# Optimization experiments

Measured on AMD Instinct MI355X. Metric: run time of the kernel, lower is better.

## Reference

```python
import jax, jax.numpy as jnp
import numpy as np

BN_EPS = 1e-5
ALPHA = 0.3
NEG = -9e9
BN_SCALE = 1.0 / np.sqrt(1.0 + BN_EPS)  # eval BatchNorm with running_mean=0, running_var=1


def gat_layer(x, mask, W, a, bn_g, bn_b, concat):
    # x: [B,N,Fin], mask: [B,N,N] bool, W: [Fin,Fo], a: [2*Fo]
    h = jnp.einsum('bnf,fo->bno', x, W)               # [B,N,Fo]
    Fo = W.shape[1]
    s1 = h @ a[:Fo]                                    # [B,N]
    s2 = h @ a[Fo:]                                    # [B,N]
    # additive decomposition of concat([h_i, h_j]) @ a (identical math)
    e = jax.nn.leaky_relu(s1[:, :, None] + s2[:, None, :], ALPHA)  # [B,N,N]
    att = jax.nn.softmax(jnp.where(mask, e, NEG), axis=-1)
    hp = jnp.einsum('bnm,bmo->bno', att, h)            # [B,N,Fo]
    # BatchNorm1d(nodes_num) in eval mode, per-node-channel affine
    hp = hp * BN_SCALE * bn_g[None, :, None] + bn_b[None, :, None]
    return jax.nn.elu(hp) if concat else hp


def setup_inputs() -> dict:
    key = jax.random.key(0)
    ks = jax.random.split(key, 10)
    B, N, F, Fo, H, C = 128, 200, 768, 32, 8, 2
    Fh = Fo * H
    return {
        'feat_matrix': jax.random.normal(ks[0], (B, N, F), jnp.float32),
        'adj': jax.random.randint(ks[1], (B, N, N), 0, 2, jnp.int32),
        'W_heads': jax.random.normal(ks[2], (H, F, Fo), jnp.float32) * 0.05,
        'a_heads': jax.random.normal(ks[3], (H, 2 * Fo), jnp.float32) * 0.1,
        'bnh_g': jnp.ones((H, N), jnp.float32),
        'bnh_b': jnp.zeros((H, N), jnp.float32),
        'bnt_g': jnp.ones((N,), jnp.float32),
        'bnt_b': jnp.zeros((N,), jnp.float32),
        'W_sent': jax.random.normal(ks[4], (Fh, C), jnp.float32) * 0.1,
        'a_sent': jax.random.normal(ks[5], (2 * C,), jnp.float32) * 0.1,
        'bns_g': jnp.ones((N,), jnp.float32),
        'bns_b': jnp.zeros((N,), jnp.float32),
        'W_para': jax.random.normal(ks[6], (Fh, C), jnp.float32) * 0.1,
        'a_para': jax.random.normal(ks[7], (2 * C,), jnp.float32) * 0.1,
        'bnp_g': jnp.ones((N,), jnp.float32),
        'bnp_b': jnp.zeros((N,), jnp.float32),
        'W_q': jax.random.normal(ks[8], (Fh, Fo), jnp.float32) * 0.1,
        'a_q': jax.random.normal(ks[9], (2 * Fo,), jnp.float32) * 0.1,
        'bnq_g': jnp.ones((N,), jnp.float32),
        'bnq_b': jnp.zeros((N,), jnp.float32),
        'W2': jax.random.normal(jax.random.fold_in(key, 99), (Fo, 2), jnp.float32) * 0.1,
    }


def reference(feat_matrix, adj, W_heads, a_heads, bnh_g, bnh_b, bnt_g, bnt_b,
              W_sent, a_sent, bns_g, bns_b, W_para, a_para, bnp_g, bnp_b,
              W_q, a_q, bnq_g, bnq_b, W2):
    mask = adj > 0
    # 8 attention heads (concat=True), vmapped over head dim
    heads = jax.vmap(lambda W, a, g, b: gat_layer(feat_matrix, mask, W, a, g, b, True))(
        W_heads, a_heads, bnh_g, bnh_b)              # [H,B,N,Fo]
    H, B, N, Fo = heads.shape
    x = jnp.moveaxis(heads, 0, 2).reshape(B, N, H * Fo)  # head-major concat, matches torch.cat
    # top-level BatchNorm1d (eval) + dropout(no-op)
    x = x * BN_SCALE * bnt_g[None, :, None] + bnt_b[None, :, None]
    logits_sent = jax.nn.sigmoid(gat_layer(x, mask, W_sent, a_sent, bns_g, bns_b, False))
    logits_para = jax.nn.elu(gat_layer(x, mask, W_para, a_para, bnp_g, bnp_b, False))
    q = gat_layer(x, mask, W_q, a_q, bnq_g, bnq_b, False)[:, 0, :]   # [B,Fo]
    logits_Qtype = jax.nn.elu(q @ W2).reshape(-1, 2)
    return (logits_sent, logits_para, logits_Qtype)
```

## Files before the change

### kernel.cpp

```cpp
#include <hip/hip_runtime.h>
#include <hip/hip_bf16.h>
#include <cstdint>

#define BN_SCALEF 0.99999500003749975f
#define EXP_SHIFT 4.0f


typedef _Float16 half8 __attribute__((ext_vector_type(8)));
typedef _Float16 half4 __attribute__((ext_vector_type(4)));
typedef float floatx4 __attribute__((ext_vector_type(4)));


__global__ __launch_bounds__(256) void prep(const int* __restrict__ adj,
                                            const float* __restrict__ W_heads,
                                            const float* __restrict__ Ws_in,
                                            const float* __restrict__ Wp_in,
                                            const float* __restrict__ Wq_in,
                                            const float* __restrict__ a_sent,
                                            const float* __restrict__ a_para,
                                            const float* __restrict__ a_q,
                                            unsigned int* __restrict__ maskw,
                                            _Float16* __restrict__ Bt,
                                            _Float16* __restrict__ W2t48) {
    int blk = blockIdx.x;
    int t = threadIdx.x;
    if (blk < 1600) {
        int w = t >> 6, lane = t & 63;
        for (int task = w; task < 64; task += 4) {
            int r = blk * 16 + (task >> 2);
            int c0 = (task & 3) * 64;
            int j = c0 + lane;
            bool v = (j < 200) && (adj[(size_t)r * 200 + j] > 0);
            unsigned long long m = __ballot(v ? 1 : 0);
            if (lane == 0) {
                maskw[r * 8 + (c0 >> 5)]     = (unsigned int)(m & 0xffffffffULL);
                maskw[r * 8 + (c0 >> 5) + 1] = (unsigned int)(m >> 32);
            }
        }
    } else if (blk < 1792) {
        __shared__ float ld[32][36];
        int blk2 = blk - 1600;
        int h = blk2 / 24, f0 = (blk2 % 24) * 32;
        int idx = t * 4;
        int fr = idx >> 5, o0 = idx & 31;
        float4 v = *(const float4*)&W_heads[(size_t)h * 24576 + (size_t)(f0 + fr) * 32 + o0];
        ld[fr][o0] = v.x; ld[fr][o0 + 1] = v.y; ld[fr][o0 + 2] = v.z; ld[fr][o0 + 3] = v.w;
        __syncthreads();
        int o = idx >> 5, fr0 = idx & 31;
        half4 hv;
#pragma unroll
        for (int u = 0; u < 4; ++u) hv[u] = (_Float16)ld[fr0 + u][o];
        *(half4*)&Bt[(size_t)(h * 32 + o) * 768 + f0 + fr0] = hv;
    } else {
        int k = t;
        for (int c = 0; c < 36; ++c) {
            float v;
            if (c < 2)      v = Ws_in[k * 2 + c];
            else if (c < 4) v = Wp_in[k * 2 + (c - 2)];
            else            v = Wq_in[k * 32 + (c - 4)];
            W2t48[c * 256 + k] = (_Float16)v;
        }
        W2t48[36 * 256 + k] = (_Float16)(Ws_in[k * 2] * a_sent[0] + Ws_in[k * 2 + 1] * a_sent[1]);
        W2t48[37 * 256 + k] = (_Float16)(Ws_in[k * 2] * a_sent[2] + Ws_in[k * 2 + 1] * a_sent[3]);
        W2t48[38 * 256 + k] = (_Float16)(Wp_in[k * 2] * a_para[0] + Wp_in[k * 2 + 1] * a_para[1]);
        W2t48[39 * 256 + k] = (_Float16)(Wp_in[k * 2] * a_para[2] + Wp_in[k * 2 + 1] * a_para[3]);
        float q1 = 0.f, q2 = 0.f;
#pragma unroll
        for (int o = 0; o < 32; ++o) {
            q1 += Wq_in[k * 32 + o] * a_q[o];
            q2 += Wq_in[k * 32 + o] * a_q[32 + o];
        }
        W2t48[40 * 256 + k] = (_Float16)q1;
        W2t48[41 * 256 + k] = (_Float16)q2;
        for (int c = 42; c < 48; ++c) W2t48[c * 256 + k] = (_Float16)0.f;
    }
}


__global__ __launch_bounds__(512) void gemm1_mfma(const float* __restrict__ A,
                                                  const _Float16* __restrict__ Bt,
                                                  _Float16* __restrict__ h16) {
    __shared__ __align__(16) _Float16 As[64 * 40];
    __shared__ __align__(16) _Float16 Bs[256 * 40];
    int t = threadIdx.x;
    int m0 = blockIdx.x * 64;
    int w = t >> 6, lane = t & 63;
    int wr = w >> 2, wc = w & 3;
    int quad = lane >> 4, l16 = lane & 15;

    floatx4 acc[2][4];
#pragma unroll
    for (int i = 0; i < 2; ++i)
#pragma unroll
        for (int j = 0; j < 4; ++j) acc[i][j] = (floatx4){0.f, 0.f, 0.f, 0.f};

    int arow = t >> 3, ako = (t & 7) * 4;
    int bcol = t >> 1, bko = (t & 1) * 16;
    const float*    Aptr = &A[(size_t)(m0 + arow) * 768 + ako];
    const _Float16* Bptr = &Bt[(size_t)bcol * 768 + bko];

    float4 pa  = *(const float4*)(Aptr);
    uint4  pb0 = *(const uint4*)(Bptr);
    uint4  pb1 = *(const uint4*)(Bptr + 8);

    for (int k0 = 0; k0 < 768; k0 += 32) {
        half4 ah;
        ah[0] = (_Float16)pa.x; ah[1] = (_Float16)pa.y;
        ah[2] = (_Float16)pa.z; ah[3] = (_Float16)pa.w;
        *(half4*)&As[arow * 40 + ako] = ah;
        *(uint4*)&Bs[bcol * 40 + bko]     = pb0;
        *(uint4*)&Bs[bcol * 40 + bko + 8] = pb1;
        __syncthreads();
        if (k0 + 32 < 768) {
            pa  = *(const float4*)(Aptr + k0 + 32);
            pb0 = *(const uint4*)(Bptr + k0 + 32);
            pb1 = *(const uint4*)(Bptr + k0 + 40);
        }
        half8 af[2], bf[4];
#pragma unroll
        for (int rt = 0; rt < 2; ++rt)
            af[rt] = *(half8*)&As[(wr * 32 + rt * 16 + l16) * 40 + quad * 8];
#pragma unroll
        for (int ct = 0; ct < 4; ++ct)
            bf[ct] = *(half8*)&Bs[(wc * 64 + ct * 16 + l16) * 40 + quad * 8];
#pragma unroll
        for (int rt = 0; rt < 2; ++rt)
#pragma unroll
            for (int ct = 0; ct < 4; ++ct)
                acc[rt][ct] = __builtin_amdgcn_mfma_f32_16x16x32_f16(af[rt], bf[ct], acc[rt][ct], 0, 0, 0);
        __syncthreads();
    }

    int rbase = m0 + wr * 32;
    int cbase = wc * 64;
#pragma unroll
    for (int rt = 0; rt < 2; ++rt)
#pragma unroll
        for (int ct = 0; ct < 4; ++ct) {
            int gc = cbase + ct * 16 + l16;
#pragma unroll
            for (int r = 0; r < 4; ++r) {
                int gr = rbase + rt * 16 + quad * 4 + r;
                h16[(size_t)gr * 256 + gc] = (_Float16)acc[rt][ct][r];
            }
        }
}


__global__ __launch_bounds__(256) void attn_heads_mfma(
    const _Float16* __restrict__ h16,
    const float* __restrict__ a_h,
    const unsigned int* __restrict__ maskw,
    const float* __restrict__ bnh_g, const float* __restrict__ bnh_b,
    const float* __restrict__ bnt_g, const float* __restrict__ bnt_b,
    _Float16* __restrict__ x16h) {
    __shared__ __align__(16) _Float16 Bs[48 * 228];
    __shared__ __align__(16) _Float16 Ps[64 * 228];
    __shared__ float s1s[256], s2s[256];
    int hb = blockIdx.x;
    int h = hb >> 7, b = hb & 127;
    int t = threadIdx.x;

    unsigned long long* bz = (unsigned long long*)Bs;
    for (int idx = t; idx < (48 * 228) / 4; idx += 256) bz[idx] = 0ULL;
    __syncthreads();
    for (int idx = t; idx < 800; idx += 256) {
        int j = idx >> 2, w8 = (idx & 3) * 8;
        half8 v = *(const half8*)&h16[(size_t)(b * 200 + j) * 256 + h * 32 + w8];
#pragma unroll
        for (int u = 0; u < 8; ++u) Bs[(w8 + u) * 228 + j] = v[u];
    }
    if (t < 200) Bs[32 * 228 + t] = (_Float16)1.0f;
    __syncthreads();

    if (t < 200) {
        float acc1 = 0.f, acc2 = 0.f;
        const float* ab = &a_h[h * 64];
#pragma unroll
        for (int o = 0; o < 32; ++o) {
            float hv = (float)Bs[o * 228 + t];
            acc1 += hv * ab[o];
            acc2 += hv * ab[32 + o];
        }
        s1s[t] = acc1; s2s[t] = acc2;
    } else {
        s1s[t] = 0.f; s2s[t] = 0.f;
    }
    __syncthreads();

    int w = t >> 6, lane = t & 63;
    int l16 = lane & 15, quad = lane >> 4;
    _Float16* Pw = &Ps[w * 16 * 228];

    int j0 = lane * 4;
    float4 s2r = *(const float4*)&s2s[j0];
    const unsigned int* mbase = &maskw[(size_t)(b * 200) * 8 + (lane >> 3)];

    for (int tile = w; tile < 13; tile += 4) {
        int i_base = tile * 16;
        unsigned int mw = mbase[(size_t)i_base * 8];
        for (int r16 = 0; r16 < 16; ++r16) {
            int i = i_base + r16;
            unsigned int mw_next = 0;
            if (r16 < 15) {
                int in = i + 1; in = in < 200 ? in : 199;
                mw_next = mbase[(size_t)in * 8];
            }
            float s1v = s1s[i];
            half4 pv;
#pragma unroll
            for (int q = 0; q < 4; ++q) {
                float e = s1v + ((const float*)&s2r)[q];
                e = fmaxf(e, 0.3f * e);
                float p = ((mw >> ((j0 + q) & 31)) & 1u) ? __expf(e - EXP_SHIFT) : 0.f;
                pv[q] = (_Float16)p;
            }
            if (j0 < 228) *(half4*)&Pw[r16 * 228 + j0] = pv;
            mw = mw_next;
        }
        floatx4 acc0 = {0.f, 0.f, 0.f, 0.f};
        floatx4 acc1 = {0.f, 0.f, 0.f, 0.f};
        floatx4 acc2 = {0.f, 0.f, 0.f, 0.f};
#pragma unroll
        for (int kt = 0; kt < 7; ++kt) {
            half8 af = *(half8*)&Pw[l16 * 228 + kt * 32 + quad * 8];
            half8 b0 = *(half8*)&Bs[(l16) * 228 + kt * 32 + quad * 8];
            half8 b1 = *(half8*)&Bs[(16 + l16) * 228 + kt * 32 + quad * 8];
            half8 b2 = *(half8*)&Bs[(32 + l16) * 228 + kt * 32 + quad * 8];
            acc0 = __builtin_amdgcn_mfma_f32_16x16x32_f16(af, b0, acc0, 0, 0, 0);
            acc1 = __builtin_amdgcn_mfma_f32_16x16x32_f16(af, b1, acc1, 0, 0, 0);
            acc2 = __builtin_amdgcn_mfma_f32_16x16x32_f16(af, b2, acc2, 0, 0, 0);
        }
#pragma unroll
        for (int r = 0; r < 4; ++r) {
            int i = i_base + quad * 4 + r;
            float rsum = __shfl(acc2[r], (lane & 48), 64);
            if (i < 200) {
                float inv = 1.f / rsum;
                float g1 = BN_SCALEF * bnh_g[h * 200 + i], c1 = bnh_b[h * 200 + i];
                float g2 = BN_SCALEF * bnt_g[i], c2 = bnt_b[i];
                float v0 = acc0[r] * inv * g1 + c1;
                v0 = v0 > 0.f ? v0 : __expf(v0) - 1.f;
                v0 = v0 * g2 + c2;
                float v1 = acc1[r] * inv * g1 + c1;
                v1 = v1 > 0.f ? v1 : __expf(v1) - 1.f;
                v1 = v1 * g2 + c2;
                size_t base = (size_t)h * 819200 + (size_t)(b * 200 + i) * 32;
                x16h[base + l16]      = (_Float16)v0;
                x16h[base + 16 + l16] = (_Float16)v1;
            }
        }
    }
}


__global__ __launch_bounds__(256) void gemm2m(const _Float16* __restrict__ Xh,
                                              const _Float16* __restrict__ Wt,
                                              float* __restrict__ H2p) {
    __shared__ __align__(16) _Float16 Xs[64 * 264];
    __shared__ __align__(16) _Float16 Ws[48 * 264];
    int t = threadIdx.x;
    int m0 = blockIdx.x * 64;
    int srow = t >> 2, schunk = (t & 3) * 8;
#pragma unroll
    for (int h = 0; h < 8; ++h) {
        half8 v = *(const half8*)&Xh[(size_t)h * 819200 + (size_t)(m0 + srow) * 32 + schunk];
        *(half8*)&Xs[srow * 264 + h * 32 + schunk] = v;
    }
#pragma unroll
    for (int p = 0; p < 6; ++p) {
        int g = t + 256 * p;
        int n = g >> 5, ko = (g & 31) * 8;
        *(half8*)&Ws[n * 264 + ko] = *(const half8*)&Wt[(size_t)n * 256 + ko];
    }
    __syncthreads();

    int w = t >> 6, lane = t & 63;
    int l16 = lane & 15, quad = lane >> 4;
    int rbase = w * 16;
    floatx4 acc[3];
#pragma unroll
    for (int c = 0; c < 3; ++c) acc[c] = (floatx4){0.f, 0.f, 0.f, 0.f};
#pragma unroll
    for (int kt = 0; kt < 8; ++kt) {
        half8 af = *(half8*)&Xs[(rbase + l16) * 264 + kt * 32 + quad * 8];
#pragma unroll
        for (int ct = 0; ct < 3; ++ct) {
            half8 bf = *(half8*)&Ws[(ct * 16 + l16) * 264 + kt * 32 + quad * 8];
            acc[ct] = __builtin_amdgcn_mfma_f32_16x16x32_f16(af, bf, acc[ct], 0, 0, 0);
        }
    }
#pragma unroll
    for (int ct = 0; ct < 3; ++ct) {
        int col = ct * 16 + l16;
#pragma unroll
        for (int r = 0; r < 4; ++r) {
            int row = m0 + rbase + quad * 4 + r;
            H2p[(size_t)row * 48 + col] = acc[ct][r];
        }
    }
}


__global__ __launch_bounds__(256) void attn_spq(const float* __restrict__ H2p,
                                                const unsigned int* __restrict__ maskw,
                                                const float* __restrict__ bns_g, const float* __restrict__ bns_b,
                                                const float* __restrict__ bnp_g, const float* __restrict__ bnp_b,
                                                const float* __restrict__ bnq_g, const float* __restrict__ bnq_b,
                                                const float* __restrict__ W2, float* __restrict__ out) {
    int b = blockIdx.x;
    int t = threadIdx.x;
    if (blockIdx.y == 2) {
        __shared__ float p_lds[200];
        __shared__ float redd[4];
        __shared__ float red2[256];
        float s1v = H2p[(size_t)(b * 200) * 48 + 40];
        float p = 0.f;
        if (t < 200) {
            unsigned int mw = maskw[(size_t)(b * 200) * 8 + (t >> 5)];
            if ((mw >> (t & 31)) & 1u) {
                float x = s1v + H2p[(size_t)(b * 200 + t) * 48 + 41];
                x = fmaxf(x, 0.3f * x);
                p = __expf(x - EXP_SHIFT);
            }
            p_lds[t] = p;
        }
        float ds = p;
        for (int off = 32; off; off >>= 1) ds += __shfl_xor(ds, off, 64);
        if ((t & 63) == 0) redd[t >> 6] = ds;
        __syncthreads();
        ds = redd[0] + redd[1] + redd[2] + redd[3];
        int o = t & 31, g = t >> 5;
        float acc = 0.f;
        for (int j = g; j < 200; j += 8)
            acc += p_lds[j] * H2p[(size_t)(b * 200 + j) * 48 + 4 + o];
        red2[t] = acc;
        __syncthreads();
        if (t < 32) {
            float s = 0.f;
#pragma unroll
            for (int gg = 0; gg < 8; ++gg) s += red2[gg * 32 + t];
            float qv = (s / ds) * (BN_SCALEF * bnq_g[0]) + bnq_b[0];
            float c0 = qv * W2[t * 2], c1 = qv * W2[t * 2 + 1];
#pragma unroll
            for (int off = 16; off; off >>= 1) {
                c0 += __shfl_xor(c0, off, 64);
                c1 += __shfl_xor(c1, off, 64);
            }
            if (t == 0) {
                out[102400 + b * 2 + 0] = c0 > 0.f ? c0 : __expf(c0) - 1.f;
                out[102400 + b * 2 + 1] = c1 > 0.f ? c1 : __expf(c1) - 1.f;
            }
        }
        return;
    }
    __shared__ float s2s[200], s2p[200];
    __shared__ float s1sA[200], s1pA[200];
    __shared__ __align__(16) float hsp[200 * 4];
    int chunk = blockIdx.y;
    if (t < 200) {
        const float* hr = &H2p[(size_t)(b * 200 + t) * 48];
        float4 hv = *(const float4*)hr;
        *(float4*)&hsp[t * 4] = hv;
        s1sA[t] = hr[36]; s2s[t] = hr[37];
        s1pA[t] = hr[38]; s2p[t] = hr[39];
    }
    __syncthreads();
    int w = t >> 6, lane = t & 63;
    for (int it = 0; it < 25; ++it) {
        int i = chunk * 100 + it * 4 + w;
        float s1sv = s1sA[i];
        float s1pv = s1pA[i];
        float ds = 0.f, dp = 0.f, pa0 = 0.f, pa1 = 0.f, pb0 = 0.f, pb1 = 0.f;
#pragma unroll
        for (int q = 0; q < 4; ++q) {
            int j = lane + 64 * q;
            if (j < 200) {
                unsigned int mw = maskw[(size_t)(b * 200 + i) * 8 + (j >> 5)];
                if ((mw >> (j & 31)) & 1u) {
                    float x1 = s1sv + s2s[j]; x1 = fmaxf(x1, 0.3f * x1);
                    float x2 = s1pv + s2p[j]; x2 = fmaxf(x2, 0.3f * x2);
                    float p1 = __expf(x1 - EXP_SHIFT), p2 = __expf(x2 - EXP_SHIFT);
                    ds += p1; dp += p2;
                    float4 hv = *(float4*)&hsp[j * 4];
                    pa0 += p1 * hv.x; pa1 += p1 * hv.y;
                    pb0 += p2 * hv.z; pb1 += p2 * hv.w;
                }
            }
        }
        for (int off = 32; off; off >>= 1) {
            ds  += __shfl_xor(ds, off, 64);  dp  += __shfl_xor(dp, off, 64);
            pa0 += __shfl_xor(pa0, off, 64); pa1 += __shfl_xor(pa1, off, 64);
            pb0 += __shfl_xor(pb0, off, 64); pb1 += __shfl_xor(pb1, off, 64);
        }
        if (lane == 0) {
            float gs = BN_SCALEF * bns_g[i], bs = bns_b[i];
            float v0 = (pa0 / ds) * gs + bs, v1 = (pa1 / ds) * gs + bs;
            out[(size_t)(b * 200 + i) * 2 + 0] = 1.f / (1.f + __expf(-v0));
            out[(size_t)(b * 200 + i) * 2 + 1] = 1.f / (1.f + __expf(-v1));
            float gp = BN_SCALEF * bnp_g[i], bp = bnp_b[i];
            float u0 = (pb0 / dp) * gp + bp, u1 = (pb1 / dp) * gp + bp;
            out[51200 + (size_t)(b * 200 + i) * 2 + 0] = u0 > 0.f ? u0 : __expf(u0) - 1.f;
            out[51200 + (size_t)(b * 200 + i) * 2 + 1] = u1 > 0.f ? u1 : __expf(u1) - 1.f;
        }
    }
}


extern "C" void kernel_launch(void* const* d_in, const int* in_sizes, int n_in,
                              void* d_out, int out_size, void* d_ws, size_t ws_size,
                              hipStream_t stream) {
    (void)in_sizes; (void)n_in; (void)out_size; (void)ws_size;
    const float* feat    = (const float*)d_in[0];
    const int*   adj     = (const int*)d_in[1];
    const float* W_heads = (const float*)d_in[2];
    const float* a_heads = (const float*)d_in[3];
    const float* bnh_g   = (const float*)d_in[4];
    const float* bnh_b   = (const float*)d_in[5];
    const float* bnt_g   = (const float*)d_in[6];
    const float* bnt_b   = (const float*)d_in[7];
    const float* W_sent  = (const float*)d_in[8];
    const float* a_sent  = (const float*)d_in[9];
    const float* bns_g   = (const float*)d_in[10];
    const float* bns_b   = (const float*)d_in[11];
    const float* W_para  = (const float*)d_in[12];
    const float* a_para  = (const float*)d_in[13];
    const float* bnp_g   = (const float*)d_in[14];
    const float* bnp_b   = (const float*)d_in[15];
    const float* W_q     = (const float*)d_in[16];
    const float* a_q     = (const float*)d_in[17];
    const float* bnq_g   = (const float*)d_in[18];
    const float* bnq_b   = (const float*)d_in[19];
    const float* W2      = (const float*)d_in[20];
    float* out = (float*)d_out;
    float* ws  = (float*)d_ws;

    _Float16* h16   = (_Float16*)ws;
    _Float16* x16h  = (_Float16*)(ws + 3276800);
    _Float16* W2t48 = (_Float16*)(ws + 6553600);
    _Float16* Bt    = (_Float16*)(ws + 6559744);
    unsigned int* maskw = (unsigned int*)(ws + 6658048);
    float* H2p   = ws + 6862848;

    prep<<<dim3(1793), dim3(256), 0, stream>>>(adj, W_heads, W_sent, W_para, W_q,
                                               a_sent, a_para, a_q, maskw, Bt, W2t48);
    gemm1_mfma<<<dim3(400), dim3(512), 0, stream>>>(feat, Bt, h16);
    attn_heads_mfma<<<dim3(1024), dim3(256), 0, stream>>>(h16, a_heads, maskw,
                                                          bnh_g, bnh_b, bnt_g, bnt_b, x16h);
    gemm2m<<<dim3(400), dim3(256), 0, stream>>>(x16h, W2t48, H2p);
    attn_spq<<<dim3(128, 3), dim3(256), 0, stream>>>(H2p, maskw, bns_g, bns_b,
                                                     bnp_g, bnp_b, bnq_g, bnq_b, W2, out);
}
```

Measured before the change: 280.2 us.

## Restructure gemm1 to stage full A rows in LDS and stream B from global

The first projection GEMM now loads a whole 32x768 slab of A into shared memory once, converting it to fp16, with a single barrier instead of a barrier per k-step. Each wave reads its B fragments directly from global memory into registers, prefetched one step ahead, so B is no longer staged through shared memory. The block shrinks to 256 threads and 32 rows, and the grid doubles to 800 blocks to raise occupancy and parallelism. In exchange, each block rereads B from global/L2, which raises cache traffic, and the larger LDS footprint (about 50KB) may limit how many blocks fit per CU.

New measurement: 296.4 us. 1.06x slower.

```diff
diff --git a/kernel.cpp b/kernel.cpp
--- a/kernel.cpp
+++ b/kernel.cpp
@@ -77,16 +77,31 @@
 }
 
 
-__global__ __launch_bounds__(512) void gemm1_mfma(const float* __restrict__ A,
+__global__ __launch_bounds__(256) void gemm1_mfma(const float* __restrict__ A,
                                                   const _Float16* __restrict__ Bt,
                                                   _Float16* __restrict__ h16) {
-    __shared__ __align__(16) _Float16 As[64 * 40];
-    __shared__ __align__(16) _Float16 Bs[256 * 40];
+    __shared__ __align__(16) _Float16 As[32 * 776];
     int t = threadIdx.x;
-    int m0 = blockIdx.x * 64;
+    int m0 = blockIdx.x * 32;
+
+    {
+        int row = t >> 3, kb = (t & 7) * 4;
+        const float* ap = &A[(size_t)(m0 + row) * 768 + kb];
+        _Float16* lp = &As[row * 776 + kb];
+#pragma unroll
+        for (int j = 0; j < 24; ++j) {
+            float4 v = *(const float4*)(ap + j * 32);
+            half4 hv;
+            hv[0] = (_Float16)v.x; hv[1] = (_Float16)v.y;
+            hv[2] = (_Float16)v.z; hv[3] = (_Float16)v.w;
+            *(half4*)(lp + j * 32) = hv;
+        }
+    }
+    __syncthreads();
+
     int w = t >> 6, lane = t & 63;
-    int wr = w >> 2, wc = w & 3;
-    int quad = lane >> 4, l16 = lane & 15;
+    int l16 = lane & 15, quad = lane >> 4;
+    int c0 = w * 64;
 
     floatx4 acc[2][4];
 #pragma unroll
@@ -94,53 +109,42 @@
 #pragma unroll
         for (int j = 0; j < 4; ++j) acc[i][j] = (floatx4){0.f, 0.f, 0.f, 0.f};
 
-    int arow = t >> 3, ako = (t & 7) * 4;
-    int bcol = t >> 1, bko = (t & 1) * 16;
-    const float*    Aptr = &A[(size_t)(m0 + arow) * 768 + ako];
-    const _Float16* Bptr = &Bt[(size_t)bcol * 768 + bko];
-
-    float4 pa  = *(const float4*)(Aptr);
-    uint4  pb0 = *(const uint4*)(Bptr);
-    uint4  pb1 = *(const uint4*)(Bptr + 8);
-
+    const _Float16* bbase = &Bt[(size_t)(c0 + l16) * 768 + quad * 8];
+
+    half8 nb[4];
+#pragma unroll
+    for (int ct = 0; ct < 4; ++ct)
+        nb[ct] = *(const half8*)(bbase + (size_t)ct * 12288);
+
+#pragma unroll 4
     for (int k0 = 0; k0 < 768; k0 += 32) {
-        half4 ah;
-        ah[0] = (_Float16)pa.x; ah[1] = (_Float16)pa.y;
-        ah[2] = (_Float16)pa.z; ah[3] = (_Float16)pa.w;
-        *(half4*)&As[arow * 40 + ako] = ah;
-        *(uint4*)&Bs[bcol * 40 + bko]     = pb0;
-        *(uint4*)&Bs[bcol * 40 + bko + 8] = pb1;
-        __syncthreads();
-        if (k0 + 32 < 768) {
-            pa  = *(const float4*)(Aptr + k0 + 32);
-            pb0 = *(const uint4*)(Bptr + k0 + 32);
-            pb1 = *(const uint4*)(Bptr + k0 + 40);
-        }
-        half8 af[2], bf[4];
-#pragma unroll
-        for (int rt = 0; rt < 2; ++rt)
-            af[rt] = *(half8*)&As[(wr * 32 + rt * 16 + l16) * 40 + quad * 8];
+        half8 bf0 = nb[0], bf1 = nb[1], bf2 = nb[2], bf3 = nb[3];
+        int kn = (k0 + 32 < 768) ? (k0 + 32) : 0;
 #pragma unroll
         for (int ct = 0; ct < 4; ++ct)
-            bf[ct] = *(half8*)&Bs[(wc * 64 + ct * 16 + l16) * 40 + quad * 8];
-#pragma unroll
-        for (int rt = 0; rt < 2; ++rt)
-#pragma unroll
-            for (int ct = 0; ct < 4; ++ct)
-                acc[rt][ct] = __builtin_amdgcn_mfma_f32_16x16x32_f16(af[rt], bf[ct], acc[rt][ct], 0, 0, 0);
-        __syncthreads();
-    }
-
-    int rbase = m0 + wr * 32;
-    int cbase = wc * 64;
+            nb[ct] = *(const half8*)(bbase + (size_t)ct * 12288 + kn);
+
+        half8 af0 = *(half8*)&As[l16 * 776 + k0 + quad * 8];
+        half8 af1 = *(half8*)&As[(16 + l16) * 776 + k0 + quad * 8];
+
+        acc[0][0] = __builtin_amdgcn_mfma_f32_16x16x32_f16(af0, bf0, acc[0][0], 0, 0, 0);
+        acc[1][0] = __builtin_amdgcn_mfma_f32_16x16x32_f16(af1, bf0, acc[1][0], 0, 0, 0);
+        acc[0][1] = __builtin_amdgcn_mfma_f32_16x16x32_f16(af0, bf1, acc[0][1], 0, 0, 0);
+        acc[1][1] = __builtin_amdgcn_mfma_f32_16x16x32_f16(af1, bf1, acc[1][1], 0, 0, 0);
+        acc[0][2] = __builtin_amdgcn_mfma_f32_16x16x32_f16(af0, bf2, acc[0][2], 0, 0, 0);
+        acc[1][2] = __builtin_amdgcn_mfma_f32_16x16x32_f16(af1, bf2, acc[1][2], 0, 0, 0);
+        acc[0][3] = __builtin_amdgcn_mfma_f32_16x16x32_f16(af0, bf3, acc[0][3], 0, 0, 0);
+        acc[1][3] = __builtin_amdgcn_mfma_f32_16x16x32_f16(af1, bf3, acc[1][3], 0, 0, 0);
+    }
+
 #pragma unroll
     for (int rt = 0; rt < 2; ++rt)
 #pragma unroll
         for (int ct = 0; ct < 4; ++ct) {
-            int gc = cbase + ct * 16 + l16;
+            int gc = c0 + ct * 16 + l16;
 #pragma unroll
             for (int r = 0; r < 4; ++r) {
-                int gr = rbase + rt * 16 + quad * 4 + r;
+                int gr = m0 + rt * 16 + quad * 4 + r;
                 h16[(size_t)gr * 256 + gc] = (_Float16)acc[rt][ct][r];
             }
         }
@@ -444,7 +448,7 @@
 
     prep<<<dim3(1793), dim3(256), 0, stream>>>(adj, W_heads, W_sent, W_para, W_q,
                                                a_sent, a_para, a_q, maskw, Bt, W2t48);
-    gemm1_mfma<<<dim3(400), dim3(512), 0, stream>>>(feat, Bt, h16);
+    gemm1_mfma<<<dim3(800), dim3(256), 0, stream>>>(feat, Bt, h16);
     attn_heads_mfma<<<dim3(1024), dim3(256), 0, stream>>>(h16, a_heads, maskw,
                                                           bnh_g, bnh_b, bnt_g, bnt_b, x16h);
     gemm2m<<<dim3(400), dim3(256), 0, stream>>>(x16h, W2t48, H2p);
```
